# Optimization experiments

Measured on AMD Instinct MI355X. Metric: run time of the kernel, lower is better.

## Reference

```python
import jax, jax.numpy as jnp
import numpy as np

B, N, D, U = 8, 2048, 512, 128


def setup_inputs() -> dict:
    key = jax.random.key(0)
    k_x, k_q, k_k, k_v, k_o = jax.random.split(key, 5)
    scale_in = 1.0 / np.sqrt(D)
    scale_u = 1.0 / np.sqrt(U)
    return {
        "inputs": jax.random.normal(k_x, (B, N, D), dtype=jnp.float32),
        "W_q": jax.random.normal(k_q, (D, U), dtype=jnp.float32) * scale_in,
        "W_k": jax.random.normal(k_k, (D, U), dtype=jnp.float32) * scale_in,
        "W_v": jax.random.normal(k_v, (D, U), dtype=jnp.float32) * scale_in,
        "W_o": jax.random.normal(k_o, (U, D), dtype=jnp.float32) * scale_u,
        "b_o": jnp.zeros((D,), dtype=jnp.float32),
    }


def reference(inputs, W_q, W_k, W_v, W_o, b_o):
    # Single-head scaled dot-product self-attention + output dense + residual
    Q = jnp.einsum('bnd,du->bnu', inputs, W_q)
    K = jnp.einsum('bnd,du->bnu', inputs, W_k)
    V = jnp.einsum('bnd,du->bnu', inputs, W_v)
    inv_sqrt_u = 1.0 / jnp.sqrt(jnp.asarray(W_q.shape[-1], inputs.dtype))
    scores = jnp.einsum('bnu,bmu->bnm', Q, K) * inv_sqrt_u  # [B,N,N]
    attn = jax.nn.softmax(scores, axis=-1)
    ctx = jnp.einsum('bnm,bmu->bnu', attn, V)  # [B,N,U]
    return jnp.einsum('bnu,ud->bnd', ctx, W_o) + b_o + inputs
```

## Files before the change

kernel.cpp:

```cpp
#include <hip/hip_runtime.h>

#define BB 8
#define NN 2048
#define DD 512
#define UU 128
#define SPLITS 4
#define KSPLIT 512

typedef __bf16 bf16_t;
typedef __bf16 bf16x4 __attribute__((ext_vector_type(4)));
typedef __bf16 bf16x8 __attribute__((ext_vector_type(8)));
typedef float floatx4 __attribute__((ext_vector_type(4)));
typedef float floatx16 __attribute__((ext_vector_type(16)));

__device__ __forceinline__ floatx4 mfma16(bf16x8 a, bf16x8 b, floatx4 c) {
  return __builtin_amdgcn_mfma_f32_16x16x32_bf16(a, b, c, 0, 0, 0);
}
__device__ __forceinline__ floatx16 mfma32(bf16x8 a, bf16x8 b, floatx16 c) {
  return __builtin_amdgcn_mfma_f32_32x32x16_bf16(a, b, c, 0, 0, 0);
}

__device__ __forceinline__ unsigned int pk2(float a, float b) {
  union { bf16_t x[2]; unsigned int u; } t;
  t.x[0] = (bf16_t)a; t.x[1] = (bf16_t)b;
  return t.u;
}

#define SW(r, g) ((((g) ^ ((r) & 7)) * 8))

__device__ __forceinline__ void gld_lds16(const bf16_t* g, bf16_t* l) {
  __builtin_amdgcn_global_load_lds(
      (const __attribute__((address_space(1))) unsigned int*)g,
      (__attribute__((address_space(3))) unsigned int*)l, 16, 0, 0);
}

__global__ __launch_bounds__(256) void cast_x_kernel(const float* __restrict__ x,
                                                     bf16_t* __restrict__ xb) {
  int G = blockIdx.x * 256 + threadIdx.x;
  int token = G >> 6;
  int g = G & 63;
  int dstg = (g & 56) | ((g & 7) ^ (token & 7));
  const float4* src = reinterpret_cast<const float4*>(x) + (size_t)G * 2;
  float4 a = src[0], b = src[1];
  bf16x8 o;
  o[0] = (bf16_t)a.x; o[1] = (bf16_t)a.y; o[2] = (bf16_t)a.z; o[3] = (bf16_t)a.w;
  o[4] = (bf16_t)b.x; o[5] = (bf16_t)b.y; o[6] = (bf16_t)b.z; o[7] = (bf16_t)b.w;
  *reinterpret_cast<bf16x8*>(&xb[(size_t)token * 512 + dstg * 8]) = o;
}

__global__ __launch_bounds__(256) void pack_w_kernel(const float* __restrict__ wq,
                                                     const float* __restrict__ wk,
                                                     const float* __restrict__ wv,
                                                     const float* __restrict__ wo,
                                                     bf16_t* __restrict__ wqkvt,
                                                     bf16_t* __restrict__ wot) {
  int gid = blockIdx.x * 256 + threadIdx.x;
  if (gid < 384 * 512) {
    int nrow = gid >> 9;
    int kdst = gid & 511;
    int ksrc = (kdst & ~56) | (((((kdst >> 3) & 7)) ^ (nrow & 7)) << 3);
    const float* src = (nrow < 128) ? wq : ((nrow < 256) ? wk : wv);
    int n = nrow & 127;
    wqkvt[gid] = (bf16_t)src[ksrc * 128 + n];
  } else {
    int g = gid - 384 * 512;
    int nrow = g >> 7;
    int kdst = g & 127;
    int ksrc = (kdst & ~56) | (((((kdst >> 3) & 7)) ^ (nrow & 7)) << 3);
    wot[g] = (bf16_t)wo[ksrc * 512 + nrow];
  }
}

__global__ __launch_bounds__(256, 4) void qkv_gemm_kernel(const bf16_t* __restrict__ xb,
                                                          const bf16_t* __restrict__ wqkvt,
                                                          bf16_t* __restrict__ Q,
                                                          bf16_t* __restrict__ K,
                                                          bf16_t* __restrict__ Vt) {
  __shared__ bf16_t lA[128 * 64];
  __shared__ bf16_t lB[64 * 64];
  const int lid = (blockIdx.x & 7) * 96 + (blockIdx.x >> 3);
  const int m0 = (lid / 6) * 128;
  const int n0 = (lid % 6) * 64;
  const int tid = threadIdx.x;
  const int w = tid >> 6, lane = tid & 63;
  const int quad = lane >> 4, l15 = lane & 15;

  floatx4 zero4 = {0.f, 0.f, 0.f, 0.f};
  floatx4 acc[2][4];
#pragma unroll
  for (int mi = 0; mi < 2; mi++)
#pragma unroll
    for (int nt = 0; nt < 4; nt++) acc[mi][nt] = zero4;

  for (int kc = 0; kc < 512; kc += 64) {
    __syncthreads();
#pragma unroll
    for (int i = 0; i < 4; i++) {
      int t = tid + i * 256;
      int r = t >> 3, g = t & 7;
      gld_lds16(&xb[(size_t)(m0 + r) * 512 + kc + g * 8], &lA[t * 8]);
    }
#pragma unroll
    for (int i = 0; i < 2; i++) {
      int t = tid + i * 256;
      int r = t >> 3, g = t & 7;
      gld_lds16(&wqkvt[(size_t)(n0 + r) * 512 + kc + g * 8], &lB[t * 8]);
    }
    asm volatile("s_waitcnt vmcnt(0)" ::: "memory");
    __syncthreads();
#pragma unroll
    for (int kb = 0; kb < 2; kb++) {
      bf16x8 bfr[4];
#pragma unroll
      for (int nt = 0; nt < 4; nt++)
        bfr[nt] = *reinterpret_cast<const bf16x8*>(
            &lB[(nt * 16 + l15) * 64 + SW(l15, kb * 4 + quad)]);
#pragma unroll
      for (int mi = 0; mi < 2; mi++) {
        bf16x8 a = *reinterpret_cast<const bf16x8*>(
            &lA[(w * 32 + mi * 16 + l15) * 64 + SW(l15, kb * 4 + quad)]);
#pragma unroll
        for (int nt = 0; nt < 4; nt++)
          acc[mi][nt] = mfma16(a, bfr[nt], acc[mi][nt]);
      }
    }
  }

#pragma unroll
  for (int mi = 0; mi < 2; mi++)
#pragma unroll
    for (int nt = 0; nt < 4; nt++) {
      int n = n0 + nt * 16 + l15;
#pragma unroll
      for (int r = 0; r < 4; r++) {
        int token = m0 + w * 32 + mi * 16 + quad * 4 + r;
        bf16_t h = (bf16_t)acc[mi][nt][r];
        if (n < 128) {
          Q[(size_t)token * 128 + n] = h;
        } else if (n < 256) {
          int nk = n - 128;
          int nsw = (nk & ~56) | ((((nk >> 3) & 7) ^ (token & 7)) << 3);
          K[(size_t)token * 128 + nsw] = h;
        } else {
          int bidx = token >> 11;
          int t = token & 2047;
          int u = n - 256;
          int tsw = (t & ~56) | ((((t >> 3) & 7) ^ (u & 7)) << 3);
          Vt[((size_t)bidx * 128 + u) * 2048 + tsw] = h;
        }
      }
    }
}

__global__ __launch_bounds__(256, 2) void attn_kernel(const bf16_t* __restrict__ Q,
                                                      const bf16_t* __restrict__ K,
                                                      const bf16_t* __restrict__ Vt,
                                                      bf16_t* __restrict__ Op,
                                                      float* __restrict__ ml) {
  __shared__ bf16_t lK[2][64 * 128];
  __shared__ bf16_t lV[2][128 * 64];

  const int lid = (blockIdx.x & 7) * 64 + (blockIdx.x >> 3);
  const int qb = lid & 15;
  const int bs = lid >> 4;
  const int b = bs >> 2;
  const int s = bs & 3;
  const int tid = threadIdx.x;
  const int w = tid >> 6, lane = tid & 63;
  const int l31 = lane & 31, h = lane >> 5;
  const float c = 0.08838834764831845f * 1.4426950408889634f;

  bf16x8 qf[8];
  {
    const bf16_t* qrow =
        &Q[((size_t)b * NN + qb * 128 + w * 32 + l31) * 128 + h * 8];
#pragma unroll
    for (int kb = 0; kb < 8; kb++)
      qf[kb] = *reinterpret_cast<const bf16x8*>(qrow + kb * 16);
  }

  float l_part = 0.f;
  floatx16 accO[4];
#pragma unroll
  for (int ut = 0; ut < 4; ut++)
#pragma unroll
    for (int i = 0; i < 16; i++) accO[ut][i] = 0.f;

  const int kt0 = s * KSPLIT;
  const bf16_t* kbase = &K[(size_t)b * NN * 128];
  const bf16_t* vbase = &Vt[(size_t)b * 128 * 2048];

  {
    const bf16_t* ksrc = kbase + (size_t)kt0 * 128;
#pragma unroll
    for (int i = 0; i < 4; i++) {
      int t = tid + i * 256;
      gld_lds16(ksrc + (size_t)t * 8, &lK[0][t * 8]);
    }
#pragma unroll
    for (int i = 0; i < 4; i++) {
      int t = tid + i * 256;
      int r = t >> 3, g = t & 7;
      gld_lds16(vbase + (size_t)r * 2048 + kt0 + g * 8, &lV[0][t * 8]);
    }
  }
  asm volatile("s_waitcnt vmcnt(0)" ::: "memory");
  __syncthreads();

  int cur = 0;
  for (int kt = kt0; kt < kt0 + KSPLIT; kt += 64) {
    if (kt + 64 < kt0 + KSPLIT) {
      const int nxt = kt + 64;
      const bf16_t* ksrc = kbase + (size_t)nxt * 128;
#pragma unroll
      for (int i = 0; i < 4; i++) {
        int t = tid + i * 256;
        gld_lds16(ksrc + (size_t)t * 8, &lK[cur ^ 1][t * 8]);
      }
#pragma unroll
      for (int i = 0; i < 4; i++) {
        int t = tid + i * 256;
        int r = t >> 3, g = t & 7;
        gld_lds16(vbase + (size_t)r * 2048 + nxt + g * 8, &lV[cur ^ 1][t * 8]);
      }
    }

    floatx16 accS[2];
#pragma unroll
    for (int km = 0; km < 2; km++)
#pragma unroll
      for (int i = 0; i < 16; i++) accS[km][i] = 0.f;

    __builtin_amdgcn_s_setprio(1);
#pragma unroll
    for (int kb = 0; kb < 8; kb++) {
#pragma unroll
      for (int km = 0; km < 2; km++) {
        int r = km * 32 + l31;
        bf16x8 kf = *reinterpret_cast<const bf16x8*>(
            &lK[cur][r * 128 + SW(r, kb * 2 + h)]);
        accS[km] = mfma32(kf, qf[kb], accS[km]);
      }
    }
    __builtin_amdgcn_s_setprio(0);

    bf16x8 pa[4];
#pragma unroll
    for (int km = 0; km < 2; km++) {
      float p[16];
#pragma unroll
      for (int i = 0; i < 16; i++) {
        p[i] = __builtin_amdgcn_exp2f(accS[km][i] * c);
        l_part += p[i];
      }
#pragma unroll
      for (int s2 = 0; s2 < 2; s2++) {
        unsigned int w00 = pk2(p[8 * s2 + 0], p[8 * s2 + 1]);
        unsigned int w01 = pk2(p[8 * s2 + 2], p[8 * s2 + 3]);
        unsigned int w10 = pk2(p[8 * s2 + 4], p[8 * s2 + 5]);
        unsigned int w11 = pk2(p[8 * s2 + 6], p[8 * s2 + 7]);
        unsigned int s0 = h ? w00 : w10;
        unsigned int s1 = h ? w01 : w11;
        unsigned int r0 = __shfl_xor(s0, 32);
        unsigned int r1 = __shfl_xor(s1, 32);
        union { unsigned int u[4]; bf16x8 v; } af;
        af.u[0] = h ? r0 : w00;
        af.u[1] = h ? r1 : w01;
        af.u[2] = h ? w10 : r0;
        af.u[3] = h ? w11 : r1;
        pa[km * 2 + s2] = af.v;
      }
    }

    __builtin_amdgcn_s_setprio(1);
#pragma unroll
    for (int ut = 0; ut < 4; ut++) {
#pragma unroll
      for (int ks = 0; ks < 4; ks++) {
        int ur = ut * 32 + l31;
        bf16x8 vf = *reinterpret_cast<const bf16x8*>(
            &lV[cur][ur * 64 + SW(ur, ks * 2 + h)]);
        accO[ut] = mfma32(pa[ks], vf, accO[ut]);
      }
    }
    __builtin_amdgcn_s_setprio(0);

    asm volatile("s_waitcnt vmcnt(0)" ::: "memory");
    __syncthreads();
    cur ^= 1;
  }

  l_part += __shfl_xor(l_part, 32);

  size_t base = ((size_t)(b * 16 + qb) * SPLITS + s);
  bf16_t* op = Op + base * (128 * 128);
#pragma unroll
  for (int ut = 0; ut < 4; ut++)
#pragma unroll
    for (int i = 0; i < 16; i++) {
      int qr = w * 32 + (i & 3) + 8 * (i >> 2) + 4 * h;
      op[qr * 128 + ut * 32 + l31] = (bf16_t)accO[ut][i];
    }
  if (h == 0) ml[base * 128 + w * 32 + l31] = l_part;
}

__global__ __launch_bounds__(256) void merge_kernel(const bf16_t* __restrict__ Op,
                                                    const float* __restrict__ ml,
                                                    bf16_t* __restrict__ ctx) {
  const int blk = blockIdx.x;
  const int qloc = blockIdx.y * 16 + (threadIdx.x >> 4);
  const int g = threadIdx.x & 15;

  float L = 0.f;
  float o[8];
#pragma unroll
  for (int j = 0; j < 8; j++) o[j] = 0.f;
#pragma unroll
  for (int s = 0; s < SPLITS; s++) {
    size_t e = (size_t)blk * SPLITS + s;
    L += ml[e * 128 + qloc];
    bf16x8 ch = *reinterpret_cast<const bf16x8*>(&Op[(e * 128 + qloc) * 128 + g * 8]);
#pragma unroll
    for (int j = 0; j < 8; j++) o[j] += (float)ch[j];
  }
  float inv = 1.0f / L;
  int gsw = (g & 8) | ((g & 7) ^ (qloc & 7));
  bf16x8 ch;
#pragma unroll
  for (int j = 0; j < 8; j++) ch[j] = (bf16_t)(o[j] * inv);
  const int bb = blk >> 4, qbl = blk & 15;
  *reinterpret_cast<bf16x8*>(
      &ctx[((size_t)bb * NN + qbl * 128 + qloc) * 128 + gsw * 8]) = ch;
}

__global__ __launch_bounds__(256, 4) void out_gemm_kernel(const bf16_t* __restrict__ ctx,
                                                          const bf16_t* __restrict__ wot,
                                                          const float* __restrict__ bo,
                                                          const float* __restrict__ x0,
                                                          float* __restrict__ out) {
  __shared__ bf16_t lA[64 * 128];
  __shared__ bf16_t lB[64 * 128];
  const int lid = (blockIdx.x & 7) * 256 + (blockIdx.x >> 3);
  const int m0 = (lid >> 3) * 64;
  const int n0 = (lid & 7) * 64;
  const int tid = threadIdx.x;
  const int w = tid >> 6, lane = tid & 63;
  const int quad = lane >> 4, l15 = lane & 15;

#pragma unroll
  for (int i = 0; i < 4; i++) {
    int t = tid + i * 256;
    gld_lds16(&ctx[(size_t)m0 * 128 + t * 8], &lA[t * 8]);
    gld_lds16(&wot[(size_t)n0 * 128 + t * 8], &lB[t * 8]);
  }
  asm volatile("s_waitcnt vmcnt(0)" ::: "memory");
  __syncthreads();

  floatx4 zero4 = {0.f, 0.f, 0.f, 0.f};
  floatx4 acc[4];
#pragma unroll
  for (int nt = 0; nt < 4; nt++) acc[nt] = zero4;
#pragma unroll
  for (int kb = 0; kb < 4; kb++) {
    bf16x8 a = *reinterpret_cast<const bf16x8*>(&lA[(w * 16 + l15) * 128 + SW(l15, kb * 4 + quad)]);
#pragma unroll
    for (int nt = 0; nt < 4; nt++) {
      bf16x8 bfr = *reinterpret_cast<const bf16x8*>(&lB[(nt * 16 + l15) * 128 + SW(l15, kb * 4 + quad)]);
      acc[nt] = mfma16(a, bfr, acc[nt]);
    }
  }

#pragma unroll
  for (int nt = 0; nt < 4; nt++) {
    int n = n0 + nt * 16 + l15;
    float bias = bo[n];
#pragma unroll
    for (int r = 0; r < 4; r++) {
      size_t m = m0 + w * 16 + quad * 4 + r;
      out[m * 512 + n] = acc[nt][r] + bias + x0[m * 512 + n];
    }
  }
}

extern "C" void kernel_launch(void* const* d_in, const int* in_sizes, int n_in,
                              void* d_out, int out_size, void* d_ws, size_t ws_size,
                              hipStream_t stream) {
  const float* x  = (const float*)d_in[0];
  const float* wq = (const float*)d_in[1];
  const float* wk = (const float*)d_in[2];
  const float* wv = (const float*)d_in[3];
  const float* wo = (const float*)d_in[4];
  const float* bo = (const float*)d_in[5];
  float* out = (float*)d_out;

  char* ws = (char*)d_ws;
  bf16_t* Qb    = (bf16_t*)(ws);
  bf16_t* Kb    = (bf16_t*)(ws + 4194304);
  bf16_t* Vt    = (bf16_t*)(ws + 2 * 4194304);
  bf16_t* Ctx   = (bf16_t*)(ws + 3 * 4194304);
  bf16_t* Wqkvt = (bf16_t*)(ws + 4 * 4194304);
  bf16_t* Wot   = (bf16_t*)(ws + 4 * 4194304 + 393216);
  bf16_t* Xb    = (bf16_t*)(ws + 4 * 4194304 + 524288);
  bf16_t* Op    = (bf16_t*)(ws + 4 * 4194304 + 524288);
  float*  ml    = (float*)(ws + 4 * 4194304 + 524288 + 33554432);

  cast_x_kernel<<<4096, 256, 0, stream>>>(x, Xb);
  pack_w_kernel<<<1024, 256, 0, stream>>>(wq, wk, wv, wo, Wqkvt, Wot);
  qkv_gemm_kernel<<<768, 256, 0, stream>>>(Xb, Wqkvt, Qb, Kb, Vt);
  attn_kernel<<<512, 256, 0, stream>>>(Qb, Kb, Vt, Op, ml);
  merge_kernel<<<dim3(128, 8), 256, 0, stream>>>(Op, ml, Ctx);
  out_gemm_kernel<<<2048, 256, 0, stream>>>(Ctx, Wot, bo, x, out);
}
```

Measured before the change: 146.8 us.

## Fuse split-merge into output GEMM and merge cast/pack prep kernels

Merges the cast_x and pack_w kernels into one prep launch. Folds the split-K attention merge into the output projection GEMM: each 512-thread block reduces the partial outputs for 64 query rows directly into LDS, loads the full W_o^T (128 KB) into LDS, and computes all 512 output columns. This removes the Ctx round trip through global memory and two launches. In exchange it uses only 256 blocks with one block per CU and a large LDS footprint, so parallelism and latency hiding are reduced.

New measurement: 143.7 us. 1.02x faster.

```diff
diff --git a/kernel.cpp b/kernel.cpp
--- a/kernel.cpp
+++ b/kernel.cpp
@@ -34,40 +34,41 @@
       (__attribute__((address_space(3))) unsigned int*)l, 16, 0, 0);
 }
 
-__global__ __launch_bounds__(256) void cast_x_kernel(const float* __restrict__ x,
-                                                     bf16_t* __restrict__ xb) {
-  int G = blockIdx.x * 256 + threadIdx.x;
-  int token = G >> 6;
-  int g = G & 63;
-  int dstg = (g & 56) | ((g & 7) ^ (token & 7));
-  const float4* src = reinterpret_cast<const float4*>(x) + (size_t)G * 2;
-  float4 a = src[0], b = src[1];
-  bf16x8 o;
-  o[0] = (bf16_t)a.x; o[1] = (bf16_t)a.y; o[2] = (bf16_t)a.z; o[3] = (bf16_t)a.w;
-  o[4] = (bf16_t)b.x; o[5] = (bf16_t)b.y; o[6] = (bf16_t)b.z; o[7] = (bf16_t)b.w;
-  *reinterpret_cast<bf16x8*>(&xb[(size_t)token * 512 + dstg * 8]) = o;
-}
-
-__global__ __launch_bounds__(256) void pack_w_kernel(const float* __restrict__ wq,
-                                                     const float* __restrict__ wk,
-                                                     const float* __restrict__ wv,
-                                                     const float* __restrict__ wo,
-                                                     bf16_t* __restrict__ wqkvt,
-                                                     bf16_t* __restrict__ wot) {
-  int gid = blockIdx.x * 256 + threadIdx.x;
-  if (gid < 384 * 512) {
-    int nrow = gid >> 9;
-    int kdst = gid & 511;
-    int ksrc = (kdst & ~56) | (((((kdst >> 3) & 7)) ^ (nrow & 7)) << 3);
-    const float* src = (nrow < 128) ? wq : ((nrow < 256) ? wk : wv);
-    int n = nrow & 127;
-    wqkvt[gid] = (bf16_t)src[ksrc * 128 + n];
+__global__ __launch_bounds__(256) void prep_kernel(const float* __restrict__ x,
+                                                   const float* __restrict__ wq,
+                                                   const float* __restrict__ wk,
+                                                   const float* __restrict__ wv,
+                                                   const float* __restrict__ wo,
+                                                   bf16_t* __restrict__ xb,
+                                                   bf16_t* __restrict__ wqkvt,
+                                                   bf16_t* __restrict__ wot) {
+  if (blockIdx.x < 4096) {
+    int G = blockIdx.x * 256 + threadIdx.x;
+    int token = G >> 6;
+    int g = G & 63;
+    int dstg = (g & 56) | ((g & 7) ^ (token & 7));
+    const float4* src = reinterpret_cast<const float4*>(x) + (size_t)G * 2;
+    float4 a = src[0], b = src[1];
+    bf16x8 o;
+    o[0] = (bf16_t)a.x; o[1] = (bf16_t)a.y; o[2] = (bf16_t)a.z; o[3] = (bf16_t)a.w;
+    o[4] = (bf16_t)b.x; o[5] = (bf16_t)b.y; o[6] = (bf16_t)b.z; o[7] = (bf16_t)b.w;
+    *reinterpret_cast<bf16x8*>(&xb[(size_t)token * 512 + dstg * 8]) = o;
   } else {
-    int g = gid - 384 * 512;
-    int nrow = g >> 7;
-    int kdst = g & 127;
-    int ksrc = (kdst & ~56) | (((((kdst >> 3) & 7)) ^ (nrow & 7)) << 3);
-    wot[g] = (bf16_t)wo[ksrc * 512 + nrow];
+    int gid = (blockIdx.x - 4096) * 256 + threadIdx.x;
+    if (gid < 384 * 512) {
+      int nrow = gid >> 9;
+      int kdst = gid & 511;
+      int ksrc = (kdst & ~56) | (((((kdst >> 3) & 7)) ^ (nrow & 7)) << 3);
+      const float* src = (nrow < 128) ? wq : ((nrow < 256) ? wk : wv);
+      int n = nrow & 127;
+      wqkvt[gid] = (bf16_t)src[ksrc * 128 + n];
+    } else {
+      int g = gid - 384 * 512;
+      int nrow = g >> 7;
+      int kdst = g & 127;
+      int ksrc = (kdst & ~56) | (((((kdst >> 3) & 7)) ^ (nrow & 7)) << 3);
+      wot[g] = (bf16_t)wo[ksrc * 512 + nrow];
+    }
   }
 }
 
@@ -304,82 +305,93 @@
   if (h == 0) ml[base * 128 + w * 32 + l31] = l_part;
 }
 
-__global__ __launch_bounds__(256) void merge_kernel(const bf16_t* __restrict__ Op,
-                                                    const float* __restrict__ ml,
-                                                    bf16_t* __restrict__ ctx) {
-  const int blk = blockIdx.x;
-  const int qloc = blockIdx.y * 16 + (threadIdx.x >> 4);
-  const int g = threadIdx.x & 15;
-
-  float L = 0.f;
-  float o[8];
-#pragma unroll
-  for (int j = 0; j < 8; j++) o[j] = 0.f;
-#pragma unroll
-  for (int s = 0; s < SPLITS; s++) {
-    size_t e = (size_t)blk * SPLITS + s;
-    L += ml[e * 128 + qloc];
-    bf16x8 ch = *reinterpret_cast<const bf16x8*>(&Op[(e * 128 + qloc) * 128 + g * 8]);
-#pragma unroll
-    for (int j = 0; j < 8; j++) o[j] += (float)ch[j];
-  }
-  float inv = 1.0f / L;
-  int gsw = (g & 8) | ((g & 7) ^ (qloc & 7));
-  bf16x8 ch;
-#pragma unroll
-  for (int j = 0; j < 8; j++) ch[j] = (bf16_t)(o[j] * inv);
-  const int bb = blk >> 4, qbl = blk & 15;
-  *reinterpret_cast<bf16x8*>(
-      &ctx[((size_t)bb * NN + qbl * 128 + qloc) * 128 + gsw * 8]) = ch;
-}
-
-__global__ __launch_bounds__(256, 4) void out_gemm_kernel(const bf16_t* __restrict__ ctx,
-                                                          const bf16_t* __restrict__ wot,
-                                                          const float* __restrict__ bo,
-                                                          const float* __restrict__ x0,
-                                                          float* __restrict__ out) {
+__global__ __launch_bounds__(512, 1) void out_merge_gemm_kernel(
+    const bf16_t* __restrict__ Op, const float* __restrict__ ml,
+    const bf16_t* __restrict__ wot, const float* __restrict__ bo,
+    const float* __restrict__ x0, float* __restrict__ out) {
+  __shared__ bf16_t lW[512 * 128];
   __shared__ bf16_t lA[64 * 128];
-  __shared__ bf16_t lB[64 * 128];
-  const int lid = (blockIdx.x & 7) * 256 + (blockIdx.x >> 3);
-  const int m0 = (lid >> 3) * 64;
-  const int n0 = (lid & 7) * 64;
+
   const int tid = threadIdx.x;
   const int w = tid >> 6, lane = tid & 63;
   const int quad = lane >> 4, l15 = lane & 15;
-
-#pragma unroll
-  for (int i = 0; i < 4; i++) {
-    int t = tid + i * 256;
-    gld_lds16(&ctx[(size_t)m0 * 128 + t * 8], &lA[t * 8]);
-    gld_lds16(&wot[(size_t)n0 * 128 + t * 8], &lB[t * 8]);
-  }
+  const int m0 = blockIdx.x * 64;
+  const int b = blockIdx.x >> 5;
+  const int qb = (blockIdx.x >> 1) & 15;
+  const int half = blockIdx.x & 1;
+  const size_t ebase = ((size_t)(b * 16 + qb)) * SPLITS;
+
+#pragma unroll
+  for (int i = 0; i < 16; i++) {
+    int tg = tid + i * 512;
+    gld_lds16(&wot[(size_t)tg * 8], &lW[tg * 8]);
+  }
+
+#pragma unroll
+  for (int j = 0; j < 2; j++) {
+    int ql = j * 32 + (tid >> 4);
+    int g = tid & 15;
+    int qrow = half * 64 + ql;
+    float L = 0.f;
+    float o[8];
+#pragma unroll
+    for (int k = 0; k < 8; k++) o[k] = 0.f;
+#pragma unroll
+    for (int s = 0; s < SPLITS; s++) {
+      size_t e = ebase + s;
+      L += ml[e * 128 + qrow];
+      bf16x8 ch = *reinterpret_cast<const bf16x8*>(
+          &Op[(e * 128 + qrow) * 128 + g * 8]);
+#pragma unroll
+      for (int k = 0; k < 8; k++) o[k] += (float)ch[k];
+    }
+    float inv = 1.0f / L;
+    int gsw = (g & 8) | ((g & 7) ^ (ql & 7));
+    bf16x8 ch;
+#pragma unroll
+    for (int k = 0; k < 8; k++) ch[k] = (bf16_t)(o[k] * inv);
+    *reinterpret_cast<bf16x8*>(&lA[ql * 128 + gsw * 8]) = ch;
+  }
+
   asm volatile("s_waitcnt vmcnt(0)" ::: "memory");
   __syncthreads();
 
   floatx4 zero4 = {0.f, 0.f, 0.f, 0.f};
-  floatx4 acc[4];
-#pragma unroll
-  for (int nt = 0; nt < 4; nt++) acc[nt] = zero4;
+  floatx4 acc[4][4];
+#pragma unroll
+  for (int mi = 0; mi < 4; mi++)
+#pragma unroll
+    for (int nt = 0; nt < 4; nt++) acc[mi][nt] = zero4;
+
 #pragma unroll
   for (int kb = 0; kb < 4; kb++) {
-    bf16x8 a = *reinterpret_cast<const bf16x8*>(&lA[(w * 16 + l15) * 128 + SW(l15, kb * 4 + quad)]);
+    bf16x8 bfr[4];
+#pragma unroll
+    for (int nt = 0; nt < 4; nt++)
+      bfr[nt] = *reinterpret_cast<const bf16x8*>(
+          &lW[(w * 64 + nt * 16 + l15) * 128 + SW(l15, kb * 4 + quad)]);
+#pragma unroll
+    for (int mi = 0; mi < 4; mi++) {
+      bf16x8 a = *reinterpret_cast<const bf16x8*>(
+          &lA[(mi * 16 + l15) * 128 + SW(l15, kb * 4 + quad)]);
+#pragma unroll
+      for (int nt = 0; nt < 4; nt++)
+        acc[mi][nt] = mfma16(a, bfr[nt], acc[mi][nt]);
+    }
+  }
+
+#pragma unroll
+  for (int mi = 0; mi < 4; mi++)
 #pragma unroll
     for (int nt = 0; nt < 4; nt++) {
-      bf16x8 bfr = *reinterpret_cast<const bf16x8*>(&lB[(nt * 16 + l15) * 128 + SW(l15, kb * 4 + quad)]);
-      acc[nt] = mfma16(a, bfr, acc[nt]);
-    }
-  }
-
-#pragma unroll
-  for (int nt = 0; nt < 4; nt++) {
-    int n = n0 + nt * 16 + l15;
-    float bias = bo[n];
-#pragma unroll
-    for (int r = 0; r < 4; r++) {
-      size_t m = m0 + w * 16 + quad * 4 + r;
-      out[m * 512 + n] = acc[nt][r] + bias + x0[m * 512 + n];
-    }
-  }
+      int n = w * 64 + nt * 16 + l15;
+      float bias = bo[n];
+#pragma unroll
+      for (int r = 0; r < 4; r++) {
+        size_t m = m0 + mi * 16 + quad * 4 + r;
+        out[m * 512 + n] = acc[mi][nt][r] + bias + x0[m * 512 + n];
+      }
+    }
 }
 
 extern "C" void kernel_launch(void* const* d_in, const int* in_sizes, int n_in,
@@ -397,17 +409,14 @@
   bf16_t* Qb    = (bf16_t*)(ws);
   bf16_t* Kb    = (bf16_t*)(ws + 4194304);
   bf16_t* Vt    = (bf16_t*)(ws + 2 * 4194304);
-  bf16_t* Ctx   = (bf16_t*)(ws + 3 * 4194304);
   bf16_t* Wqkvt = (bf16_t*)(ws + 4 * 4194304);
   bf16_t* Wot   = (bf16_t*)(ws + 4 * 4194304 + 393216);
   bf16_t* Xb    = (bf16_t*)(ws + 4 * 4194304 + 524288);
   bf16_t* Op    = (bf16_t*)(ws + 4 * 4194304 + 524288);
   float*  ml    = (float*)(ws + 4 * 4194304 + 524288 + 33554432);
 
-  cast_x_kernel<<<4096, 256, 0, stream>>>(x, Xb);
-  pack_w_kernel<<<1024, 256, 0, stream>>>(wq, wk, wv, wo, Wqkvt, Wot);
+  prep_kernel<<<5120, 256, 0, stream>>>(x, wq, wk, wv, wo, Xb, Wqkvt, Wot);
   qkv_gemm_kernel<<<768, 256, 0, stream>>>(Xb, Wqkvt, Qb, Kb, Vt);
   attn_kernel<<<512, 256, 0, stream>>>(Qb, Kb, Vt, Op, ml);
-  merge_kernel<<<dim3(128, 8), 256, 0, stream>>>(Op, ml, Ctx);
-  out_gemm_kernel<<<2048, 256, 0, stream>>>(Ctx, Wot, bo, x, out);
-}
+  out_merge_gemm_kernel<<<256, 512, 0, stream>>>(Op, ml, Wot, bo, x, out);
+}
```
